# Optimization experiments

Hardware: AMD Instinct MI355X
Metric: run time of the kernel (lower is better)

## Reference

```python
import jax, jax.numpy as jnp
import numpy as np

DIM = 512
HID = 1024
E = 8          # num_experts
K = 2          # num_experts_per_tok
B, S = 4, 2048


def setup_inputs() -> dict:
    key = jax.random.key(0)
    ks = jax.random.split(key, 10)
    sd = DIM ** -0.5
    sh = HID ** -0.5
    return {
        "x": jax.random.normal(ks[0], (B, S, DIM), dtype=jnp.float32),
        "gate_w": jax.random.normal(ks[1], (E, DIM), dtype=jnp.float32) * sd,
        "biases": jnp.zeros((E,), dtype=jnp.float32),  # e_expert_biases
        # routed experts: swiglu  y = (silu(x@w1) * (x@w3)) @ w2
        "w1": jax.random.normal(ks[2], (E, DIM, HID), dtype=jnp.float32) * sd,
        "w3": jax.random.normal(ks[3], (E, DIM, HID), dtype=jnp.float32) * sd,
        "w2": jax.random.normal(ks[4], (E, HID, DIM), dtype=jnp.float32) * sh,
        # single shared expert
        "sw1": jax.random.normal(ks[5], (DIM, HID), dtype=jnp.float32) * sd,
        "sw3": jax.random.normal(ks[6], (DIM, HID), dtype=jnp.float32) * sd,
        "sw2": jax.random.normal(ks[7], (HID, DIM), dtype=jnp.float32) * sh,
    }


def reference(x, gate_w, biases, w1, w3, w2, sw1, sw3, sw2):
    Bb, Ss, D = x.shape
    xt = x.reshape(Bb * Ss, D)                      # [T, D]

    # shared expert (applied to full x)
    shared = (jax.nn.silu(xt @ sw1) * (xt @ sw3)) @ sw2  # [T, D]

    # router
    scores = xt @ gate_w.T                          # [T, E]
    # indices chosen from biased scores (aux-free load balancing)
    _, idx = jax.lax.top_k(scores + biases, K)      # [T, K] int
    # gate values are top-k of the UNBIASED scores (as in original code)
    topv, _ = jax.lax.top_k(scores, K)              # [T, K]
    p = jax.nn.sigmoid(topv)
    p = p / jnp.sum(p, axis=-1, keepdims=True)      # [T, K]

    # every expert on every token (dense-combine MoE reference)
    h = jax.nn.silu(jnp.einsum('td,edh->eth', xt, w1)) * jnp.einsum('td,edh->eth', xt, w3)
    y = jnp.einsum('eth,ehd->etd', h, w2)           # [E, T, D]

    onehot = jax.nn.one_hot(idx, E, dtype=xt.dtype)  # [T, K, E]
    comb = jnp.einsum('tk,tke->te', p, onehot)       # [T, E] combine weights
    out = jnp.einsum('te,etd->td', comb, y) + shared
    return out.reshape(Bb, Ss, D)
```

## Files before the change

kernel.cpp:

```cpp
#include <hip/hip_runtime.h>
#include <hip/hip_bf16.h>


#define Tn 8192
#define Dd 512
#define Hh 1024
#define NEx 9

typedef __attribute__((ext_vector_type(8))) short short8;
typedef __attribute__((ext_vector_type(4))) float f32x4;

#define AS1 __attribute__((address_space(1)))
#define AS3 __attribute__((address_space(3)))

#define OFF_XB    ((size_t)0)
#define OFF_W13T  (OFF_XB + (size_t)Tn * Dd * 2)
#define OFF_W2T   (OFF_W13T + (size_t)NEx * 2 * Hh * Dd * 2)
#define OFF_HBUF  (OFF_W2T + (size_t)NEx * Dd * Hh * 2)
#define OFF_TOK   (OFF_HBUF + (size_t)(3 * Tn) * Hh * 2)
#define OFF_SLOTP (OFF_TOK + (size_t)8 * Tn * 4)
#define OFF_PG    (OFF_SLOTP + (size_t)Tn * 2 * 4)
#define OFF_CNT   (OFF_PG + (size_t)Tn * 2 * 4)
#define OFF_OFFS  (OFF_CNT + 1024)
#define OFF_YC    OFF_XB

__device__ __forceinline__ ushort f2bf(float f) {
    unsigned int u = __float_as_uint(f);
    return (ushort)((u + 0x7fffu + ((u >> 16) & 1u)) >> 16);
}
__device__ __forceinline__ float bf2f(short s) {
    return __uint_as_float(((unsigned int)(unsigned short)s) << 16);
}

__global__ __launch_bounds__(256) void preproc_kernel(
        const float* __restrict__ x, const float* __restrict__ gw,
        const float* __restrict__ bias,
        const float* __restrict__ w1, const float* __restrict__ sw1,
        const float* __restrict__ w3, const float* __restrict__ sw3,
        const float* __restrict__ w2, const float* __restrict__ sw2,
        ushort* __restrict__ w13t, ushort* __restrict__ w2t,
        int* __restrict__ cnt, int* __restrict__ tok,
        int* __restrict__ slotp, float* __restrict__ pg,
        ushort* __restrict__ xb, int* __restrict__ off, int* __restrict__ cntc) {
    __shared__ float tile[32][33];
    __shared__ int le[64];
    __shared__ float lg[64];
    __shared__ int lpos[64];
    __shared__ int lcnt[8];
    __shared__ int gbase[8];
    int bb = blockIdx.x;
    int tid = threadIdx.x;

    if (bb >= 256) {
        int tb = bb - 256;
        int z = tb >> 9;
        int fam = z / 9, sl = z - fam * 9;
        int bxx = tb & 31, byy = (tb >> 5) & 15;
        int tx = tid & 31, ty = tid >> 5;
        if (fam < 2) {
            const float* base = (fam == 0) ? ((sl < 8) ? w1 + (size_t)sl * Dd * Hh : sw1)
                                           : ((sl < 8) ? w3 + (size_t)sl * Dd * Hh : sw3);
            ushort* dst = w13t + (size_t)sl * 2 * Hh * Dd;
            int c0 = bxx * 32, r0 = byy * 32;
#pragma unroll
            for (int k = 0; k < 4; ++k)
                tile[ty + 8 * k][tx] = base[(size_t)(r0 + ty + 8 * k) * Hh + c0 + tx];
            __syncthreads();
#pragma unroll
            for (int k = 0; k < 4; ++k) {
                int h = c0 + ty + 8 * k;
                int n = (((h >> 4) * 2 + fam) << 4) + (h & 15);
                dst[(size_t)n * Dd + r0 + tx] = f2bf(tile[tx][ty + 8 * k]);
            }
        } else {
            const float* base = (sl < 8) ? w2 + (size_t)sl * Dd * Hh : sw2;
            ushort* dst = w2t + (size_t)sl * Dd * Hh;
            int r0 = bxx * 32, c0 = byy * 32;
#pragma unroll
            for (int k = 0; k < 4; ++k)
                tile[ty + 8 * k][tx] = base[(size_t)(r0 + ty + 8 * k) * Dd + c0 + tx];
            __syncthreads();
#pragma unroll
            for (int k = 0; k < 4; ++k)
                dst[(size_t)(c0 + ty + 8 * k) * Hh + r0 + tx] = f2bf(tile[tx][ty + 8 * k]);
        }
        return;
    }

    int lane = tid & 63, wave = tid >> 6;
    if (tid < 8) lcnt[tid] = 0;
    __syncthreads();
    int t0 = bb * 32 + wave * 8;
    for (int it = 0; it < 8; ++it) {
        int t = t0 + it;
        const float4* xr = (const float4*)(x + (size_t)t * Dd);
        float4 xa = xr[lane * 2], xc = xr[lane * 2 + 1];
        ushort4 o1, o2;
        o1.x = f2bf(xa.x); o1.y = f2bf(xa.y); o1.z = f2bf(xa.z); o1.w = f2bf(xa.w);
        o2.x = f2bf(xc.x); o2.y = f2bf(xc.y); o2.z = f2bf(xc.z); o2.w = f2bf(xc.w);
        *(ushort4*)(xb + (size_t)t * Dd + lane * 8) = o1;
        *(ushort4*)(xb + (size_t)t * Dd + lane * 8 + 4) = o2;
        float sc[8];
#pragma unroll
        for (int e = 0; e < 8; ++e) {
            const float4* gr = (const float4*)(gw + (size_t)e * Dd);
            float4 ga = gr[lane * 2], gc = gr[lane * 2 + 1];
            float s = xa.x * ga.x + xa.y * ga.y + xa.z * ga.z + xa.w * ga.w
                    + xc.x * gc.x + xc.y * gc.y + xc.z * gc.z + xc.w * gc.w;
#pragma unroll
            for (int o = 32; o > 0; o >>= 1) s += __shfl_xor(s, o);
            sc[e] = s;
        }
        if (lane == 0) {
            float b0 = -1e30f; int i0 = 0;
#pragma unroll
            for (int e = 0; e < 8; ++e) { float bv = sc[e] + bias[e]; if (bv > b0) { b0 = bv; i0 = e; } }
            float b1v = -1e30f; int i1 = (i0 == 0) ? 1 : 0;
#pragma unroll
            for (int e = 0; e < 8; ++e) if (e != i0) { float bv = sc[e] + bias[e]; if (bv > b1v) { b1v = bv; i1 = e; } }
            float v0 = -1e30f; int k0i = 0;
#pragma unroll
            for (int e = 0; e < 8; ++e) if (sc[e] > v0) { v0 = sc[e]; k0i = e; }
            float v1 = -1e30f;
#pragma unroll
            for (int e = 0; e < 8; ++e) if (e != k0i && sc[e] > v1) v1 = sc[e];
            float p0 = 1.f / (1.f + __expf(-v0));
            float p1 = 1.f / (1.f + __expf(-v1));
            float inv = 1.f / (p0 + p1);
            int ai = (wave * 8 + it) * 2;
            le[ai] = i0;     lg[ai] = p0 * inv;
            le[ai + 1] = i1; lg[ai + 1] = p1 * inv;
        }
    }
    __syncthreads();
    if (tid < 64) lpos[tid] = atomicAdd(&lcnt[le[tid]], 1);
    __syncthreads();
    if (tid < 8) gbase[tid] = atomicAdd(&cnt[tid * 32], lcnt[tid]);
    __syncthreads();
    if (tid < 64) {
        int e = le[tid];
        int dst = gbase[e] + lpos[tid];
        int t = bb * 32 + (tid >> 1);
        tok[(size_t)e * Tn + dst] = t;
        slotp[t * 2 + (tid & 1)] = (e << 16) | dst;
        pg[t * 2 + (tid & 1)] = lg[tid];
    }
    __syncthreads();
    if (tid == 0) {
        __threadfence();
        if (atomicAdd(&cnt[16], 1) == 255) {
            int s = 0;
            for (int e = 0; e < 8; ++e) {
                int c = atomicAdd(&cnt[e * 32], 0);
                cntc[e] = c; off[e] = s; s += c;
            }
            off[8] = s;
            cntc[8] = Tn;
        }
    }
}

__global__ __launch_bounds__(256, 2) void stage1_kernel(
        const ushort* __restrict__ xb, const ushort* __restrict__ w13t,
        const int* __restrict__ tok, const int* __restrict__ cntc,
        const int* __restrict__ off, ushort* __restrict__ Hbuf) {
    int b = blockIdx.x;
    int xcd = b & 7, slot = b >> 3;
    int e, xblk, yblk;
    if (slot < 1024) { e = xcd; xblk = slot >> 4; yblk = slot & 15; }
    else { int s = slot - 1024; e = 8; xblk = (xcd << 3) + (s >> 4); yblk = s & 15; }
    int cn = cntc[e];
    int m0 = xblk * 128;
    if (m0 >= cn) return;
    int n0 = yblk * 128;
    const ushort* we = w13t + (size_t)e * 2 * Hh * Dd;

    __shared__ ushort As[128 * 64];
    __shared__ ushort Bs[128 * 64];
    __shared__ int toks[128];

    int tid = threadIdx.x;
    if (tid < 128) {
        int sl2 = m0 + tid;
        int sl = sl2 < cn ? sl2 : cn - 1;
        toks[tid] = (e == 8) ? sl : tok[(size_t)e * Tn + sl];
    }
    __syncthreads();

    int lane = tid & 63, wave = tid >> 6;
    int wm = (wave & 1) * 64, wn = (wave >> 1) * 64;
    int col15 = lane & 15, quad = lane >> 4;
    int lr = lane >> 3;
    int lcx = ((lane & 7) ^ lr) * 8;

    const ushort* gA[4];
    const ushort* gB[4];
#pragma unroll
    for (int i = 0; i < 4; ++i) {
        int cid = wave * 4 + i;
        gA[i] = xb + (size_t)toks[cid * 8 + lr] * Dd + lcx;
        gB[i] = we + (size_t)(n0 + cid * 8 + lr) * Dd + lcx;
    }

    f32x4 acc[4][4];
#pragma unroll
    for (int a = 0; a < 4; ++a)
#pragma unroll
        for (int b2 = 0; b2 < 4; ++b2) acc[a][b2] = (f32x4){0.f, 0.f, 0.f, 0.f};

#pragma unroll
    for (int kb = 0; kb < Dd; kb += 64) {
#pragma unroll
        for (int i = 0; i < 4; ++i)
            __builtin_amdgcn_global_load_lds((const AS1 void*)(gA[i] + kb), (AS3 void*)(As + (wave * 4 + i) * 512), 16, 0, 0);
#pragma unroll
        for (int i = 0; i < 4; ++i)
            __builtin_amdgcn_global_load_lds((const AS1 void*)(gB[i] + kb), (AS3 void*)(Bs + (wave * 4 + i) * 512), 16, 0, 0);
        __syncthreads();
#pragma unroll
        for (int ks = 0; ks < 2; ++ks) {
            int px = ((ks * 4 + quad) ^ (col15 & 7)) * 8;
            short8 a[4], b2[4];
#pragma unroll
            for (int mi = 0; mi < 4; ++mi)
                a[mi] = *(const short8*)&As[(wm + mi * 16 + col15) * 64 + px];
#pragma unroll
            for (int ni = 0; ni < 4; ++ni)
                b2[ni] = *(const short8*)&Bs[(wn + ni * 16 + col15) * 64 + px];
#pragma unroll
            for (int mi = 0; mi < 4; ++mi)
#pragma unroll
                for (int ni = 0; ni < 4; ++ni)
                    acc[mi][ni] = __builtin_amdgcn_mfma_f32_16x16x32_bf16(a[mi], b2[ni], acc[mi][ni], 0, 0, 0);
        }
        __syncthreads();
    }

    int oe = off[e];
    int hbase = (n0 + wn) >> 1;
#pragma unroll
    for (int mi = 0; mi < 4; ++mi)
#pragma unroll
        for (int r = 0; r < 4; ++r) {
            int sl2 = m0 + wm + mi * 16 + quad * 4 + r;
            if (sl2 < cn) {
                size_t rowb = (size_t)(oe + sl2) * Hh;
#pragma unroll
                for (int np = 0; np < 2; ++np) {
                    float h1 = acc[mi][np * 2][r], h3 = acc[mi][np * 2 + 1][r];
                    float s = h1 / (1.f + __expf(-h1));
                    Hbuf[rowb + hbase + np * 16 + col15] = f2bf(s * h3);
                }
            }
        }
}

__global__ __launch_bounds__(256, 3) void stage2_kernel(
        const ushort* __restrict__ Hbuf, const ushort* __restrict__ w2t,
        const int* __restrict__ cntc, const int* __restrict__ off,
        ushort* __restrict__ Yc) {
    int b = blockIdx.x;
    int xcd = b & 7, slot = b >> 3;
    int e, xblk, yblk;
    if (slot < 256) { e = xcd; xblk = slot >> 2; yblk = slot & 3; }
    else { int s = slot - 256; e = 8; xblk = (xcd << 3) + (s >> 2); yblk = s & 3; }
    int cn = cntc[e];
    int m0 = xblk * 128;
    if (m0 >= cn) return;
    int n0 = yblk * 128;
    int oe = off[e];
    const ushort* w2e = w2t + (size_t)e * Dd * Hh;

    __shared__ ushort As[128 * 64];
    __shared__ ushort Bs[128 * 64];

    int tid = threadIdx.x;
    int lane = tid & 63, wave = tid >> 6;
    int wm = (wave & 1) * 64, wn = (wave >> 1) * 64;
    int col15 = lane & 15, quad = lane >> 4;
    int lr = lane >> 3;
    int lcx = ((lane & 7) ^ lr) * 8;

    const ushort* gA[4];
    const ushort* gB[4];
#pragma unroll
    for (int i = 0; i < 4; ++i) {
        int cid = wave * 4 + i;
        gA[i] = Hbuf + (size_t)(oe + m0 + cid * 8 + lr) * Hh + lcx;
        gB[i] = w2e + (size_t)(n0 + cid * 8 + lr) * Hh + lcx;
    }

    f32x4 acc[4][4];
#pragma unroll
    for (int a = 0; a < 4; ++a)
#pragma unroll
        for (int b2 = 0; b2 < 4; ++b2) acc[a][b2] = (f32x4){0.f, 0.f, 0.f, 0.f};

#pragma unroll
    for (int kb = 0; kb < Hh; kb += 64) {
#pragma unroll
        for (int i = 0; i < 4; ++i)
            __builtin_amdgcn_global_load_lds((const AS1 void*)(gA[i] + kb), (AS3 void*)(As + (wave * 4 + i) * 512), 16, 0, 0);
#pragma unroll
        for (int i = 0; i < 4; ++i)
            __builtin_amdgcn_global_load_lds((const AS1 void*)(gB[i] + kb), (AS3 void*)(Bs + (wave * 4 + i) * 512), 16, 0, 0);
        __syncthreads();
#pragma unroll
        for (int ks = 0; ks < 2; ++ks) {
            int px = ((ks * 4 + quad) ^ (col15 & 7)) * 8;
            short8 a[4], b2[4];
#pragma unroll
            for (int mi = 0; mi < 4; ++mi)
                a[mi] = *(const short8*)&As[(wm + mi * 16 + col15) * 64 + px];
#pragma unroll
            for (int ni = 0; ni < 4; ++ni)
                b2[ni] = *(const short8*)&Bs[(wn + ni * 16 + col15) * 64 + px];
#pragma unroll
            for (int mi = 0; mi < 4; ++mi)
#pragma unroll
                for (int ni = 0; ni < 4; ++ni)
                    acc[mi][ni] = __builtin_amdgcn_mfma_f32_16x16x32_bf16(a[mi], b2[ni], acc[mi][ni], 0, 0, 0);
        }
        __syncthreads();
    }

#pragma unroll
    for (int mi = 0; mi < 4; ++mi)
#pragma unroll
        for (int r = 0; r < 4; ++r) {
            int sl2 = m0 + wm + mi * 16 + quad * 4 + r;
            if (sl2 < cn) {
                size_t rowb = (size_t)(oe + sl2) * Dd;
#pragma unroll
                for (int ni = 0; ni < 4; ++ni)
                    Yc[rowb + n0 + wn + ni * 16 + col15] = f2bf(acc[mi][ni][r]);
            }
        }
}

__global__ __launch_bounds__(256) void combine_kernel(const ushort* __restrict__ Yc,
        const int* __restrict__ slotp, const float* __restrict__ pg,
        const int* __restrict__ off, float* __restrict__ out) {
    int g = blockIdx.x * 256 + threadIdx.x;
    int t = g >> 6;
    int c = (g & 63) * 8;
    int p0 = slotp[t * 2], p1 = slotp[t * 2 + 1];
    float g0 = pg[t * 2], g1 = pg[t * 2 + 1];
    int s0 = off[p0 >> 16] + (p0 & 0xffff);
    int s1 = off[p1 >> 16] + (p1 & 0xffff);
    int s2 = off[8] + t;
    short8 a = *(const short8*)(Yc + (size_t)s0 * Dd + c);
    short8 b = *(const short8*)(Yc + (size_t)s1 * Dd + c);
    short8 d = *(const short8*)(Yc + (size_t)s2 * Dd + c);
    float o[8];
#pragma unroll
    for (int i = 0; i < 8; ++i)
        o[i] = g0 * bf2f(a[i]) + g1 * bf2f(b[i]) + bf2f(d[i]);
    float* dst = out + (size_t)t * Dd + c;
    *(float4*)dst = (float4){o[0], o[1], o[2], o[3]};
    *(float4*)(dst + 4) = (float4){o[4], o[5], o[6], o[7]};
}

extern "C" void kernel_launch(void* const* d_in, const int* in_sizes, int n_in,
                              void* d_out, int out_size, void* d_ws, size_t ws_size,
                              hipStream_t stream) {
    (void)in_sizes; (void)n_in; (void)out_size; (void)ws_size;
    const float* x    = (const float*)d_in[0];
    const float* gw   = (const float*)d_in[1];
    const float* bias = (const float*)d_in[2];
    const float* w1   = (const float*)d_in[3];
    const float* w3   = (const float*)d_in[4];
    const float* w2   = (const float*)d_in[5];
    const float* sw1  = (const float*)d_in[6];
    const float* sw3  = (const float*)d_in[7];
    const float* sw2  = (const float*)d_in[8];
    float* out = (float*)d_out;

    char* ws = (char*)d_ws;
    ushort* xb    = (ushort*)(ws + OFF_XB);
    ushort* w13t  = (ushort*)(ws + OFF_W13T);
    ushort* w2t   = (ushort*)(ws + OFF_W2T);
    ushort* Hbuf  = (ushort*)(ws + OFF_HBUF);
    ushort* Yc    = (ushort*)(ws + OFF_YC);
    int*    tok   = (int*)(ws + OFF_TOK);
    int*    slotp = (int*)(ws + OFF_SLOTP);
    float*  pg    = (float*)(ws + OFF_PG);
    int*    cnt   = (int*)(ws + OFF_CNT);
    int*    off   = (int*)(ws + OFF_OFFS);
    int*    cntc  = off + 16;

    hipMemsetAsync(cnt, 0, 1024, stream);

    preproc_kernel<<<14080, 256, 0, stream>>>(x, gw, bias, w1, sw1, w3, sw3, w2, sw2,
                                              w13t, w2t, cnt, tok, slotp, pg, xb, off, cntc);
    stage1_kernel<<<9216, 256, 0, stream>>>(xb, w13t, tok, cntc, off, Hbuf);
    stage2_kernel<<<2304, 256, 0, stream>>>(Hbuf, w2t, cntc, off, Yc);
    combine_kernel<<<2048, 256, 0, stream>>>(Yc, slotp, pg, off, out);
}
```

Before: 239.9 us.

## Widen stage2 tile to 128x256 and vectorize weight transpose loads

Stage2 now computes a 128x256 output tile per block with 8 N-subtiles per wave, halving the grid and reusing each loaded A tile across twice as many output columns. LDS grows to 48KB and the accumulators double, so launch bounds drop to 2 blocks per SM. Separately, the weight-transpose path in preproc loads float4 per thread and writes ushort4, cutting the number of memory instructions. The risks are lower occupancy and fewer blocks in stage2, plus possible LDS bank conflicts on the column reads in the transpose.

```diff
diff --git a/kernel.cpp b/kernel.cpp
--- a/kernel.cpp
+++ b/kernel.cpp
@@ -56,33 +56,36 @@
         int z = tb >> 9;
         int fam = z / 9, sl = z - fam * 9;
         int bxx = tb & 31, byy = (tb >> 5) & 15;
-        int tx = tid & 31, ty = tid >> 5;
+        int t8 = tid & 7, th = tid >> 3;
+        int tx4 = t8 * 4;
         if (fam < 2) {
             const float* base = (fam == 0) ? ((sl < 8) ? w1 + (size_t)sl * Dd * Hh : sw1)
                                            : ((sl < 8) ? w3 + (size_t)sl * Dd * Hh : sw3);
             ushort* dst = w13t + (size_t)sl * 2 * Hh * Dd;
             int c0 = bxx * 32, r0 = byy * 32;
-#pragma unroll
-            for (int k = 0; k < 4; ++k)
-                tile[ty + 8 * k][tx] = base[(size_t)(r0 + ty + 8 * k) * Hh + c0 + tx];
+            float4 v = *(const float4*)&base[(size_t)(r0 + th) * Hh + c0 + tx4];
+            tile[th][tx4] = v.x; tile[th][tx4 + 1] = v.y;
+            tile[th][tx4 + 2] = v.z; tile[th][tx4 + 3] = v.w;
             __syncthreads();
-#pragma unroll
-            for (int k = 0; k < 4; ++k) {
-                int h = c0 + ty + 8 * k;
-                int n = (((h >> 4) * 2 + fam) << 4) + (h & 15);
-                dst[(size_t)n * Dd + r0 + tx] = f2bf(tile[tx][ty + 8 * k]);
-            }
+            int h = c0 + th;
+            int n = (((h >> 4) * 2 + fam) << 4) + (h & 15);
+            ushort4 o;
+            o.x = f2bf(tile[tx4][th]);     o.y = f2bf(tile[tx4 + 1][th]);
+            o.z = f2bf(tile[tx4 + 2][th]); o.w = f2bf(tile[tx4 + 3][th]);
+            *(ushort4*)&dst[(size_t)n * Dd + r0 + tx4] = o;
         } else {
             const float* base = (sl < 8) ? w2 + (size_t)sl * Dd * Hh : sw2;
             ushort* dst = w2t + (size_t)sl * Dd * Hh;
             int r0 = bxx * 32, c0 = byy * 32;
-#pragma unroll
-            for (int k = 0; k < 4; ++k)
-                tile[ty + 8 * k][tx] = base[(size_t)(r0 + ty + 8 * k) * Dd + c0 + tx];
+            float4 v = *(const float4*)&base[(size_t)(r0 + th) * Dd + c0 + tx4];
+            tile[th][tx4] = v.x; tile[th][tx4 + 1] = v.y;
+            tile[th][tx4 + 2] = v.z; tile[th][tx4 + 3] = v.w;
             __syncthreads();
-#pragma unroll
-            for (int k = 0; k < 4; ++k)
-                dst[(size_t)(c0 + ty + 8 * k) * Hh + r0 + tx] = f2bf(tile[tx][ty + 8 * k]);
+            int d = c0 + th;
+            ushort4 o;
+            o.x = f2bf(tile[tx4][th]);     o.y = f2bf(tile[tx4 + 1][th]);
+            o.z = f2bf(tile[tx4 + 2][th]); o.w = f2bf(tile[tx4 + 3][th]);
+            *(ushort4*)&dst[(size_t)d * Hh + r0 + tx4] = o;
         }
         return;
     }
@@ -255,46 +258,46 @@
         }
 }
 
-__global__ __launch_bounds__(256, 3) void stage2_kernel(
+__global__ __launch_bounds__(256, 2) void stage2_kernel(
         const ushort* __restrict__ Hbuf, const ushort* __restrict__ w2t,
         const int* __restrict__ cntc, const int* __restrict__ off,
         ushort* __restrict__ Yc) {
     int b = blockIdx.x;
     int xcd = b & 7, slot = b >> 3;
     int e, xblk, yblk;
-    if (slot < 256) { e = xcd; xblk = slot >> 2; yblk = slot & 3; }
-    else { int s = slot - 256; e = 8; xblk = (xcd << 3) + (s >> 2); yblk = s & 3; }
+    if (slot < 128) { e = xcd; xblk = slot >> 1; yblk = slot & 1; }
+    else { int s = slot - 128; e = 8; xblk = (xcd << 3) + (s >> 1); yblk = s & 1; }
     int cn = cntc[e];
     int m0 = xblk * 128;
     if (m0 >= cn) return;
-    int n0 = yblk * 128;
+    int n0 = yblk * 256;
     int oe = off[e];
     const ushort* w2e = w2t + (size_t)e * Dd * Hh;
 
     __shared__ ushort As[128 * 64];
-    __shared__ ushort Bs[128 * 64];
+    __shared__ ushort Bs[256 * 64];
 
     int tid = threadIdx.x;
     int lane = tid & 63, wave = tid >> 6;
-    int wm = (wave & 1) * 64, wn = (wave >> 1) * 64;
+    int wm = (wave & 1) * 64, wn = (wave >> 1) * 128;
     int col15 = lane & 15, quad = lane >> 4;
     int lr = lane >> 3;
     int lcx = ((lane & 7) ^ lr) * 8;
 
     const ushort* gA[4];
-    const ushort* gB[4];
-#pragma unroll
-    for (int i = 0; i < 4; ++i) {
-        int cid = wave * 4 + i;
-        gA[i] = Hbuf + (size_t)(oe + m0 + cid * 8 + lr) * Hh + lcx;
-        gB[i] = w2e + (size_t)(n0 + cid * 8 + lr) * Hh + lcx;
-    }
-
-    f32x4 acc[4][4];
+    const ushort* gB[8];
+#pragma unroll
+    for (int i = 0; i < 4; ++i)
+        gA[i] = Hbuf + (size_t)(oe + m0 + (wave * 4 + i) * 8 + lr) * Hh + lcx;
+#pragma unroll
+    for (int i = 0; i < 8; ++i)
+        gB[i] = w2e + (size_t)(n0 + (wave * 8 + i) * 8 + lr) * Hh + lcx;
+
+    f32x4 acc[4][8];
 #pragma unroll
     for (int a = 0; a < 4; ++a)
 #pragma unroll
-        for (int b2 = 0; b2 < 4; ++b2) acc[a][b2] = (f32x4){0.f, 0.f, 0.f, 0.f};
+        for (int b2 = 0; b2 < 8; ++b2) acc[a][b2] = (f32x4){0.f, 0.f, 0.f, 0.f};
 
 #pragma unroll
     for (int kb = 0; kb < Hh; kb += 64) {
@@ -302,23 +305,23 @@
         for (int i = 0; i < 4; ++i)
             __builtin_amdgcn_global_load_lds((const AS1 void*)(gA[i] + kb), (AS3 void*)(As + (wave * 4 + i) * 512), 16, 0, 0);
 #pragma unroll
-        for (int i = 0; i < 4; ++i)
-            __builtin_amdgcn_global_load_lds((const AS1 void*)(gB[i] + kb), (AS3 void*)(Bs + (wave * 4 + i) * 512), 16, 0, 0);
+        for (int i = 0; i < 8; ++i)
+            __builtin_amdgcn_global_load_lds((const AS1 void*)(gB[i] + kb), (AS3 void*)(Bs + (wave * 8 + i) * 512), 16, 0, 0);
         __syncthreads();
 #pragma unroll
         for (int ks = 0; ks < 2; ++ks) {
             int px = ((ks * 4 + quad) ^ (col15 & 7)) * 8;
-            short8 a[4], b2[4];
+            short8 a[4], b2[8];
 #pragma unroll
             for (int mi = 0; mi < 4; ++mi)
                 a[mi] = *(const short8*)&As[(wm + mi * 16 + col15) * 64 + px];
 #pragma unroll
-            for (int ni = 0; ni < 4; ++ni)
+            for (int ni = 0; ni < 8; ++ni)
                 b2[ni] = *(const short8*)&Bs[(wn + ni * 16 + col15) * 64 + px];
 #pragma unroll
             for (int mi = 0; mi < 4; ++mi)
 #pragma unroll
-                for (int ni = 0; ni < 4; ++ni)
+                for (int ni = 0; ni < 8; ++ni)
                     acc[mi][ni] = __builtin_amdgcn_mfma_f32_16x16x32_bf16(a[mi], b2[ni], acc[mi][ni], 0, 0, 0);
         }
         __syncthreads();
@@ -332,7 +335,7 @@
             if (sl2 < cn) {
                 size_t rowb = (size_t)(oe + sl2) * Dd;
 #pragma unroll
-                for (int ni = 0; ni < 4; ++ni)
+                for (int ni = 0; ni < 8; ++ni)
                     Yc[rowb + n0 + wn + ni * 16 + col15] = f2bf(acc[mi][ni][r]);
             }
         }
@@ -394,6 +397,6 @@
     preproc_kernel<<<14080, 256, 0, stream>>>(x, gw, bias, w1, sw1, w3, sw3, w2, sw2,
                                               w13t, w2t, cnt, tok, slotp, pg, xb, off, cntc);
     stage1_kernel<<<9216, 256, 0, stream>>>(xb, w13t, tok, cntc, off, Hbuf);
-    stage2_kernel<<<2304, 256, 0, stream>>>(Hbuf, w2t, cntc, off, Yc);
+    stage2_kernel<<<1152, 256, 0, stream>>>(Hbuf, w2t, cntc, off, Yc);
     combine_kernel<<<2048, 256, 0, stream>>>(Yc, slotp, pg, off, out);
 }
```

Result: faster. 231.0 us (-3.7%).
